# Optimization experiments

Measured on AMD Instinct MI355X. Metric: run time of the kernel, lower is better.

## Reference

```python
import jax, jax.numpy as jnp
import numpy as np

E, EMB, H, MUL = 100000, 64, 128, 64
SQRT3 = 1.7320508075688772
SQRT6 = 2.449489742783178
INV_SQRT2 = 0.7071067811865476  # path normalization: 2 paths feed 0e and 1o outputs


def setup_inputs() -> dict:
    key = jax.random.key(0)
    ks = jax.random.split(key, 10)
    d = {
        "emb": jax.random.normal(ks[0], (E, EMB), jnp.float32),
        "x1": jax.random.normal(ks[1], (E, 4 * MUL), jnp.float32),   # 64x0e + 64x1o
        "x2": jax.random.normal(ks[2], (E, 4), jnp.float32),          # 1x0e + 1x1o
        "W0": jax.random.normal(ks[3], (EMB, H), jnp.float32),
        "W1": jax.random.normal(ks[4], (H, H), jnp.float32),
    }
    for i, k in enumerate(ks[5:10]):
        d[f"P{i+1}"] = jax.random.normal(k, (H, MUL), jnp.float32)
    return d


def _forward(emb, x1, x2, W0, W1, P1, P2, P3, P4, P5):
    # MLP with 1/sqrt(fan_in) normalization (e3nn haiku MultiLayerPerceptron)
    h = jax.nn.silu(emb @ W0 / jnp.sqrt(jnp.float32(EMB)))
    h = jax.nn.silu(h @ W1 / jnp.sqrt(jnp.float32(H)))            # (E, H)
    inv = 1.0 / jnp.sqrt(jnp.float32(H))                           # w.shape[0]**-0.5
    # per-instruction path weights, shape (E, MUL): einsum('x...,x->...') batched
    w1, w2, w3, w4, w5 = (h @ P * inv for P in (P1, P2, P3, P4, P5))

    x1_0 = x1[:, :MUL]                                             # (E, MUL)    0e
    x1_1 = x1[:, MUL:].reshape(E, MUL, 3)                          # (E, MUL, 3) 1o
    x2_0 = x2[:, 0]                                                # (E,)        0e
    x2_1 = x2[:, 1:4]                                              # (E, 3)      1o

    # instruction 1: 0e x 0e -> 0e   (w3j = 1)
    # instruction 4: 1o x 1o -> 0e   (w3j = delta_ij / sqrt(3))
    out_0e = INV_SQRT2 * (
        w1 * x1_0 * x2_0[:, None]
        + w4 * jnp.einsum("eui,ei->eu", x1_1, x2_1) / SQRT3
    )                                                              # (E, MUL)
    # instruction 2: 1o x 0e -> 1o ; instruction 3: 0e x 1o -> 1o
    out_1o = INV_SQRT2 * (
        w2[:, :, None] * x1_1 * x2_0[:, None, None]
        + w3[:, :, None] * x1_0[:, :, None] * x2_1[:, None, :]
    )                                                              # (E, MUL, 3)
    # instruction 5: 1o x 1o -> 1e  (w3j = eps_ijk / sqrt(6))
    out_1e = w5[:, :, None] * jnp.cross(x1_1, x2_1[:, None, :]) / SQRT6

    return jnp.concatenate(
        [out_0e, out_1o.reshape(E, 3 * MUL), out_1e.reshape(E, 3 * MUL)], axis=-1
    )                                                              # (E, 448)


def reference(emb, x1, x2, W0, W1, P1, P2, P3, P4, P5):
    return _forward(emb, x1, x2, W0, W1, P1, P2, P3, P4, P5)
```

## Files before the change

kernel.cpp:

```cpp
#include <hip/hip_runtime.h>

#define E_TOT 100000

typedef _Float16 half8   __attribute__((ext_vector_type(8)));
typedef float    float4v __attribute__((ext_vector_type(4)));

__device__ __forceinline__ float silu_f(float x) {
    return x / (1.0f + __expf(-x));
}

__global__ void prep_weights(const float* __restrict__ W0,
                             const float* __restrict__ W1,
                             const float* __restrict__ P1,
                             const float* __restrict__ P2,
                             const float* __restrict__ P3,
                             const float* __restrict__ P4,
                             const float* __restrict__ P5,
                             _Float16* __restrict__ wf)
{
    int gid  = blockIdx.x * 256 + threadIdx.x;
    int j    = gid & 7;
    int lane = (gid >> 3) & 63;
    int krow = ((lane >> 4) << 3) + j;
    int ncol = lane & 15;
    float v;
    if (gid < 8192) {
        int kt = (gid >> 9) & 1, nt = gid >> 10;
        v = W0[(kt * 32 + krow) * 128 + nt * 16 + ncol];
    } else if (gid < 24576) {
        int rem = gid - 8192;
        int kt = (rem >> 9) & 3, nt = rem >> 11;
        v = W1[(kt * 32 + krow) * 128 + nt * 16 + ncol];
    } else {
        int rem = gid - 24576;
        int kt = (rem >> 9) & 3, nt = (rem >> 11) & 3, m = rem >> 13;
        const float* Pm = (m == 0) ? P1 : (m == 1) ? P2 : (m == 2) ? P3 : (m == 3) ? P4 : P5;
        v = Pm[(kt * 32 + krow) * 64 + nt * 16 + ncol];
    }
    wf[gid] = (_Float16)v;
}

__global__ __launch_bounds__(256, 4)
void tpmlp_main(const float* __restrict__ emb,
                const float* __restrict__ x1,
                const float* __restrict__ x2,
                const _Float16* __restrict__ wf,
                float* __restrict__ out)
{
    const float INV_SQRT_EMB = 0.125f;
    const float INV_SQRT_H   = 0.08838834764831845f;
    const float INV_SQRT3    = 0.5773502691896258f;
    const float INV_SQRT6    = 0.4082482904638631f;
    const float INV_SQRT2_C  = 0.7071067811865476f;

    __shared__ _Float16 s_h[64 * 136];

    const int tid  = threadIdx.x;
    const int lane = tid & 63;
    const int wv   = tid >> 6;
    const int l15  = lane & 15;
    const int lq   = lane >> 4;
    const int e0   = blockIdx.x * 64;

    const _Float16* __restrict__ W0f = wf;
    const _Float16* __restrict__ W1f = wf + 8192;
    const _Float16* __restrict__ Pf  = wf + 24576;

    half8 a0 = {0,0,0,0,0,0,0,0}, a1 = {0,0,0,0,0,0,0,0};
    {
        int row = e0 + wv * 16 + l15;
        if (row < E_TOT) {
            const float* er = emb + (size_t)row * 64 + lq * 8;
            float4v v0 = *(const float4v*)er;
            float4v v1 = *(const float4v*)(er + 4);
            float4v v2 = *(const float4v*)(er + 32);
            float4v v3 = *(const float4v*)(er + 36);
            #pragma unroll
            for (int t = 0; t < 4; ++t) { a0[t] = (_Float16)v0[t]; a0[4+t] = (_Float16)v1[t]; }
            #pragma unroll
            for (int t = 0; t < 4; ++t) { a1[t] = (_Float16)v2[t]; a1[4+t] = (_Float16)v3[t]; }
        }
    }

    #pragma unroll
    for (int nt = 0; nt < 8; ++nt) {
        float4v c = {0.f, 0.f, 0.f, 0.f};
        half8 b0 = *(const half8*)&W0f[((nt * 2 + 0) * 64 + lane) * 8];
        half8 b1 = *(const half8*)&W0f[((nt * 2 + 1) * 64 + lane) * 8];
        c = __builtin_amdgcn_mfma_f32_16x16x32_f16(a0, b0, c, 0, 0, 0);
        c = __builtin_amdgcn_mfma_f32_16x16x32_f16(a1, b1, c, 0, 0, 0);
        #pragma unroll
        for (int r = 0; r < 4; ++r)
            s_h[(wv * 16 + lq * 4 + r) * 136 + nt * 16 + l15] =
                (_Float16)silu_f(c[r] * INV_SQRT_EMB);
    }
    __syncthreads();

    half8 a2[4];
    #pragma unroll
    for (int kt = 0; kt < 4; ++kt)
        a2[kt] = *(const half8*)&s_h[(wv * 16 + l15) * 136 + kt * 32 + lq * 8];
    __syncthreads();

    #pragma unroll
    for (int nt = 0; nt < 8; ++nt) {
        float4v c = {0.f, 0.f, 0.f, 0.f};
        #pragma unroll
        for (int kt = 0; kt < 4; ++kt) {
            half8 b = *(const half8*)&W1f[((nt * 4 + kt) * 64 + lane) * 8];
            c = __builtin_amdgcn_mfma_f32_16x16x32_f16(a2[kt], b, c, 0, 0, 0);
        }
        #pragma unroll
        for (int r = 0; r < 4; ++r)
            s_h[(wv * 16 + lq * 4 + r) * 136 + nt * 16 + l15] =
                (_Float16)silu_f(c[r] * INV_SQRT_H);
    }
    __syncthreads();

    half8 a3[4];
    #pragma unroll
    for (int kt = 0; kt < 4; ++kt)
        a3[kt] = *(const half8*)&s_h[(wv * 16 + l15) * 136 + kt * 32 + lq * 8];

    float4v acc3[5][4];
    #pragma unroll
    for (int m = 0; m < 5; ++m)
        #pragma unroll
        for (int nt = 0; nt < 4; ++nt)
            acc3[m][nt] = (float4v){0.f, 0.f, 0.f, 0.f};

    #pragma unroll
    for (int m = 0; m < 5; ++m)
        #pragma unroll
        for (int nt = 0; nt < 4; ++nt)
            #pragma unroll
            for (int kt = 0; kt < 4; ++kt) {
                half8 b = *(const half8*)&Pf[((m * 16 + nt * 4 + kt) * 64 + lane) * 8];
                acc3[m][nt] = __builtin_amdgcn_mfma_f32_16x16x32_f16(a3[kt], b, acc3[m][nt], 0, 0, 0);
            }

    #pragma unroll
    for (int r = 0; r < 4; ++r) {
        int e = e0 + wv * 16 + lq * 4 + r;
        if (e < E_TOT) {
            const float* x1p = x1 + (size_t)e * 256;
            float4v x2v = *(const float4v*)(x2 + (size_t)e * 4);
            float x20 = x2v[0], b0 = x2v[1], b1 = x2v[2], b2 = x2v[3];
            float* op = out + (size_t)e * 448;
            #pragma unroll
            for (int nt = 0; nt < 4; ++nt) {
                int u = nt * 16 + l15;
                float w1 = acc3[0][nt][r] * INV_SQRT_H;
                float w2 = acc3[1][nt][r] * INV_SQRT_H;
                float w3 = acc3[2][nt][r] * INV_SQRT_H;
                float w4 = acc3[3][nt][r] * INV_SQRT_H;
                float w5 = acc3[4][nt][r] * INV_SQRT_H;

                float x10 = x1p[u];
                float a_0 = x1p[64 + 3 * u];
                float a_1 = x1p[65 + 3 * u];
                float a_2 = x1p[66 + 3 * u];

                float dot = a_0 * b0 + a_1 * b1 + a_2 * b2;

                op[u] = INV_SQRT2_C * (w1 * x10 * x20 + w4 * dot * INV_SQRT3);

                op[64 + 3 * u] = INV_SQRT2_C * (w2 * a_0 * x20 + w3 * x10 * b0);
                op[65 + 3 * u] = INV_SQRT2_C * (w2 * a_1 * x20 + w3 * x10 * b1);
                op[66 + 3 * u] = INV_SQRT2_C * (w2 * a_2 * x20 + w3 * x10 * b2);

                op[256 + 3 * u] = w5 * (a_1 * b2 - a_2 * b1) * INV_SQRT6;
                op[257 + 3 * u] = w5 * (a_2 * b0 - a_0 * b2) * INV_SQRT6;
                op[258 + 3 * u] = w5 * (a_0 * b1 - a_1 * b0) * INV_SQRT6;
            }
        }
    }
}

extern "C" void kernel_launch(void* const* d_in, const int* in_sizes, int n_in,
                              void* d_out, int out_size, void* d_ws, size_t ws_size,
                              hipStream_t stream) {
    const float* emb = (const float*)d_in[0];
    const float* x1  = (const float*)d_in[1];
    const float* x2  = (const float*)d_in[2];
    const float* W0  = (const float*)d_in[3];
    const float* W1  = (const float*)d_in[4];
    const float* P1  = (const float*)d_in[5];
    const float* P2  = (const float*)d_in[6];
    const float* P3  = (const float*)d_in[7];
    const float* P4  = (const float*)d_in[8];
    const float* P5  = (const float*)d_in[9];

    _Float16* wf = (_Float16*)d_ws;

    prep_weights<<<dim3(256), dim3(256), 0, stream>>>(W0, W1, P1, P2, P3, P4, P5, wf);
    tpmlp_main<<<dim3((E_TOT + 63) / 64), dim3(256), 0, stream>>>(
        emb, x1, x2, wf, (float*)d_out);
}
```

Measured before the change: 320.1 us.

## Use single-wave blocks over 32 rows, reuse B fragments, nontemporal output stores

Each block becomes one 64-lane wavefront handling two 16-row tiles. Every weight fragment loaded from global memory now feeds two MFMAs instead of one, and the P-stage accumulators are restructured per output column tile to reduce live registers. Output writes switch to nontemporal stores to avoid polluting cache. Bounds checks are removed; this relies on E being divisible by 32, which holds for 100000.

```diff
diff --git a/kernel.cpp b/kernel.cpp
--- a/kernel.cpp
+++ b/kernel.cpp
@@ -40,7 +40,7 @@
     wf[gid] = (_Float16)v;
 }
 
-__global__ __launch_bounds__(256, 4)
+__global__ __launch_bounds__(64, 4)
 void tpmlp_main(const float* __restrict__ emb,
                 const float* __restrict__ x1,
                 const float* __restrict__ x2,
@@ -53,108 +53,119 @@
     const float INV_SQRT6    = 0.4082482904638631f;
     const float INV_SQRT2_C  = 0.7071067811865476f;
 
-    __shared__ _Float16 s_h[64 * 136];
-
-    const int tid  = threadIdx.x;
-    const int lane = tid & 63;
-    const int wv   = tid >> 6;
+    __shared__ _Float16 s_h[32 * 136];
+
+    const int lane = threadIdx.x;
     const int l15  = lane & 15;
     const int lq   = lane >> 4;
-    const int e0   = blockIdx.x * 64;
+    const int e0   = blockIdx.x * 32;
 
     const _Float16* __restrict__ W0f = wf;
     const _Float16* __restrict__ W1f = wf + 8192;
     const _Float16* __restrict__ Pf  = wf + 24576;
 
-    half8 a0 = {0,0,0,0,0,0,0,0}, a1 = {0,0,0,0,0,0,0,0};
-    {
-        int row = e0 + wv * 16 + l15;
-        if (row < E_TOT) {
-            const float* er = emb + (size_t)row * 64 + lq * 8;
-            float4v v0 = *(const float4v*)er;
-            float4v v1 = *(const float4v*)(er + 4);
-            float4v v2 = *(const float4v*)(er + 32);
-            float4v v3 = *(const float4v*)(er + 36);
-            #pragma unroll
-            for (int t = 0; t < 4; ++t) { a0[t] = (_Float16)v0[t]; a0[4+t] = (_Float16)v1[t]; }
-            #pragma unroll
-            for (int t = 0; t < 4; ++t) { a1[t] = (_Float16)v2[t]; a1[4+t] = (_Float16)v3[t]; }
+    half8 a0[2], a1[2];
+    #pragma unroll
+    for (int t = 0; t < 2; ++t) {
+        const float* er = emb + (size_t)(e0 + t * 16 + l15) * 64 + lq * 8;
+        float4v v0 = *(const float4v*)er;
+        float4v v1 = *(const float4v*)(er + 4);
+        float4v v2 = *(const float4v*)(er + 32);
+        float4v v3 = *(const float4v*)(er + 36);
+        #pragma unroll
+        for (int q = 0; q < 4; ++q) {
+            a0[t][q] = (_Float16)v0[q]; a0[t][4 + q] = (_Float16)v1[q];
+            a1[t][q] = (_Float16)v2[q]; a1[t][4 + q] = (_Float16)v3[q];
         }
     }
 
     #pragma unroll
     for (int nt = 0; nt < 8; ++nt) {
-        float4v c = {0.f, 0.f, 0.f, 0.f};
         half8 b0 = *(const half8*)&W0f[((nt * 2 + 0) * 64 + lane) * 8];
         half8 b1 = *(const half8*)&W0f[((nt * 2 + 1) * 64 + lane) * 8];
-        c = __builtin_amdgcn_mfma_f32_16x16x32_f16(a0, b0, c, 0, 0, 0);
-        c = __builtin_amdgcn_mfma_f32_16x16x32_f16(a1, b1, c, 0, 0, 0);
-        #pragma unroll
-        for (int r = 0; r < 4; ++r)
-            s_h[(wv * 16 + lq * 4 + r) * 136 + nt * 16 + l15] =
-                (_Float16)silu_f(c[r] * INV_SQRT_EMB);
+        #pragma unroll
+        for (int t = 0; t < 2; ++t) {
+            float4v c = {0.f, 0.f, 0.f, 0.f};
+            c = __builtin_amdgcn_mfma_f32_16x16x32_f16(a0[t], b0, c, 0, 0, 0);
+            c = __builtin_amdgcn_mfma_f32_16x16x32_f16(a1[t], b1, c, 0, 0, 0);
+            #pragma unroll
+            for (int r = 0; r < 4; ++r)
+                s_h[(t * 16 + lq * 4 + r) * 136 + nt * 16 + l15] =
+                    (_Float16)silu_f(c[r] * INV_SQRT_EMB);
+        }
     }
     __syncthreads();
 
-    half8 a2[4];
-    #pragma unroll
-    for (int kt = 0; kt < 4; ++kt)
-        a2[kt] = *(const half8*)&s_h[(wv * 16 + l15) * 136 + kt * 32 + lq * 8];
+    half8 a2[2][4];
+    #pragma unroll
+    for (int t = 0; t < 2; ++t)
+        #pragma unroll
+        for (int kt = 0; kt < 4; ++kt)
+            a2[t][kt] = *(const half8*)&s_h[(t * 16 + l15) * 136 + kt * 32 + lq * 8];
     __syncthreads();
 
     #pragma unroll
     for (int nt = 0; nt < 8; ++nt) {
-        float4v c = {0.f, 0.f, 0.f, 0.f};
-        #pragma unroll
-        for (int kt = 0; kt < 4; ++kt) {
-            half8 b = *(const half8*)&W1f[((nt * 4 + kt) * 64 + lane) * 8];
-            c = __builtin_amdgcn_mfma_f32_16x16x32_f16(a2[kt], b, c, 0, 0, 0);
+        half8 b[4];
+        #pragma unroll
+        for (int kt = 0; kt < 4; ++kt)
+            b[kt] = *(const half8*)&W1f[((nt * 4 + kt) * 64 + lane) * 8];
+        #pragma unroll
+        for (int t = 0; t < 2; ++t) {
+            float4v c = {0.f, 0.f, 0.f, 0.f};
+            #pragma unroll
+            for (int kt = 0; kt < 4; ++kt)
+                c = __builtin_amdgcn_mfma_f32_16x16x32_f16(a2[t][kt], b[kt], c, 0, 0, 0);
+            #pragma unroll
+            for (int r = 0; r < 4; ++r)
+                s_h[(t * 16 + lq * 4 + r) * 136 + nt * 16 + l15] =
+                    (_Float16)silu_f(c[r] * INV_SQRT_H);
         }
-        #pragma unroll
-        for (int r = 0; r < 4; ++r)
-            s_h[(wv * 16 + lq * 4 + r) * 136 + nt * 16 + l15] =
-                (_Float16)silu_f(c[r] * INV_SQRT_H);
     }
     __syncthreads();
 
-    half8 a3[4];
-    #pragma unroll
-    for (int kt = 0; kt < 4; ++kt)
-        a3[kt] = *(const half8*)&s_h[(wv * 16 + l15) * 136 + kt * 32 + lq * 8];
-
-    float4v acc3[5][4];
-    #pragma unroll
-    for (int m = 0; m < 5; ++m)
-        #pragma unroll
-        for (int nt = 0; nt < 4; ++nt)
-            acc3[m][nt] = (float4v){0.f, 0.f, 0.f, 0.f};
-
-    #pragma unroll
-    for (int m = 0; m < 5; ++m)
-        #pragma unroll
-        for (int nt = 0; nt < 4; ++nt)
+    half8 a3[2][4];
+    #pragma unroll
+    for (int t = 0; t < 2; ++t)
+        #pragma unroll
+        for (int kt = 0; kt < 4; ++kt)
+            a3[t][kt] = *(const half8*)&s_h[(t * 16 + l15) * 136 + kt * 32 + lq * 8];
+
+    #pragma unroll
+    for (int nt = 0; nt < 4; ++nt) {
+        float4v acc[2][5];
+        #pragma unroll
+        for (int t = 0; t < 2; ++t)
+            #pragma unroll
+            for (int m = 0; m < 5; ++m)
+                acc[t][m] = (float4v){0.f, 0.f, 0.f, 0.f};
+
+        #pragma unroll
+        for (int m = 0; m < 5; ++m)
             #pragma unroll
             for (int kt = 0; kt < 4; ++kt) {
                 half8 b = *(const half8*)&Pf[((m * 16 + nt * 4 + kt) * 64 + lane) * 8];
-                acc3[m][nt] = __builtin_amdgcn_mfma_f32_16x16x32_f16(a3[kt], b, acc3[m][nt], 0, 0, 0);
+                #pragma unroll
+                for (int t = 0; t < 2; ++t)
+                    acc[t][m] = __builtin_amdgcn_mfma_f32_16x16x32_f16(a3[t][kt], b, acc[t][m], 0, 0, 0);
             }
 
-    #pragma unroll
-    for (int r = 0; r < 4; ++r) {
-        int e = e0 + wv * 16 + lq * 4 + r;
-        if (e < E_TOT) {
-            const float* x1p = x1 + (size_t)e * 256;
-            float4v x2v = *(const float4v*)(x2 + (size_t)e * 4);
-            float x20 = x2v[0], b0 = x2v[1], b1 = x2v[2], b2 = x2v[3];
-            float* op = out + (size_t)e * 448;
-            #pragma unroll
-            for (int nt = 0; nt < 4; ++nt) {
-                int u = nt * 16 + l15;
-                float w1 = acc3[0][nt][r] * INV_SQRT_H;
-                float w2 = acc3[1][nt][r] * INV_SQRT_H;
-                float w3 = acc3[2][nt][r] * INV_SQRT_H;
-                float w4 = acc3[3][nt][r] * INV_SQRT_H;
-                float w5 = acc3[4][nt][r] * INV_SQRT_H;
+        const int u = nt * 16 + l15;
+        #pragma unroll
+        for (int t = 0; t < 2; ++t)
+            #pragma unroll
+            for (int r = 0; r < 4; ++r) {
+                const int e = e0 + t * 16 + lq * 4 + r;
+                const float* x1p = x1 + (size_t)e * 256;
+                float4v x2v = *(const float4v*)(x2 + (size_t)e * 4);
+                float x20 = x2v[0], b0 = x2v[1], b1 = x2v[2], b2 = x2v[3];
+                float* op = out + (size_t)e * 448;
+
+                float w1 = acc[t][0][r] * INV_SQRT_H;
+                float w2 = acc[t][1][r] * INV_SQRT_H;
+                float w3 = acc[t][2][r] * INV_SQRT_H;
+                float w4 = acc[t][3][r] * INV_SQRT_H;
+                float w5 = acc[t][4][r] * INV_SQRT_H;
 
                 float x10 = x1p[u];
                 float a_0 = x1p[64 + 3 * u];
@@ -163,17 +174,23 @@
 
                 float dot = a_0 * b0 + a_1 * b1 + a_2 * b2;
 
-                op[u] = INV_SQRT2_C * (w1 * x10 * x20 + w4 * dot * INV_SQRT3);
-
-                op[64 + 3 * u] = INV_SQRT2_C * (w2 * a_0 * x20 + w3 * x10 * b0);
-                op[65 + 3 * u] = INV_SQRT2_C * (w2 * a_1 * x20 + w3 * x10 * b1);
-                op[66 + 3 * u] = INV_SQRT2_C * (w2 * a_2 * x20 + w3 * x10 * b2);
-
-                op[256 + 3 * u] = w5 * (a_1 * b2 - a_2 * b1) * INV_SQRT6;
-                op[257 + 3 * u] = w5 * (a_2 * b0 - a_0 * b2) * INV_SQRT6;
-                op[258 + 3 * u] = w5 * (a_0 * b1 - a_1 * b0) * INV_SQRT6;
+                __builtin_nontemporal_store(
+                    INV_SQRT2_C * (w1 * x10 * x20 + w4 * dot * INV_SQRT3), op + u);
+
+                __builtin_nontemporal_store(
+                    INV_SQRT2_C * (w2 * a_0 * x20 + w3 * x10 * b0), op + 64 + 3 * u);
+                __builtin_nontemporal_store(
+                    INV_SQRT2_C * (w2 * a_1 * x20 + w3 * x10 * b1), op + 65 + 3 * u);
+                __builtin_nontemporal_store(
+                    INV_SQRT2_C * (w2 * a_2 * x20 + w3 * x10 * b2), op + 66 + 3 * u);
+
+                __builtin_nontemporal_store(
+                    w5 * (a_1 * b2 - a_2 * b1) * INV_SQRT6, op + 256 + 3 * u);
+                __builtin_nontemporal_store(
+                    w5 * (a_2 * b0 - a_0 * b2) * INV_SQRT6, op + 257 + 3 * u);
+                __builtin_nontemporal_store(
+                    w5 * (a_0 * b1 - a_1 * b0) * INV_SQRT6, op + 258 + 3 * u);
             }
-        }
     }
 }
 
@@ -194,6 +211,6 @@
     _Float16* wf = (_Float16*)d_ws;
 
     prep_weights<<<dim3(256), dim3(256), 0, stream>>>(W0, W1, P1, P2, P3, P4, P5, wf);
-    tpmlp_main<<<dim3((E_TOT + 63) / 64), dim3(256), 0, stream>>>(
+    tpmlp_main<<<dim3((E_TOT + 31) / 32), dim3(64), 0, stream>>>(
         emb, x1, x2, wf, (float*)d_out);
 }
```

After: 388.2 us. 1.21x slower.

## Use single-wave blocks and interleave projection MFMAs with per-tile epilogue

Applied to the files above, without the earlier changes.

Blocks shrink from four waves over 64 rows to one wave over 16 rows, so barriers only synchronize a single wave and shared memory per block drops. The projection stage now computes the five weight tiles for one column slice and immediately applies the tensor-product epilogue, cutting live accumulators from 80 to 20 registers to ease register pressure and occupancy limits. x2 values are prefetched at kernel start. Bounds checks are removed, which is valid because 100000 divides by 16. The trade-off is four times as many blocks and per-wave reloads of the shared weight fragments.

```diff
diff --git a/kernel.cpp b/kernel.cpp
--- a/kernel.cpp
+++ b/kernel.cpp
@@ -40,7 +40,7 @@
     wf[gid] = (_Float16)v;
 }
 
-__global__ __launch_bounds__(256, 4)
+__global__ __launch_bounds__(64, 4)
 void tpmlp_main(const float* __restrict__ emb,
                 const float* __restrict__ x1,
                 const float* __restrict__ x2,
@@ -53,45 +53,46 @@
     const float INV_SQRT6    = 0.4082482904638631f;
     const float INV_SQRT2_C  = 0.7071067811865476f;
 
-    __shared__ _Float16 s_h[64 * 136];
+    __shared__ _Float16 s_h[16 * 136];
 
-    const int tid  = threadIdx.x;
-    const int lane = tid & 63;
-    const int wv   = tid >> 6;
+    const int lane = threadIdx.x;
     const int l15  = lane & 15;
     const int lq   = lane >> 4;
-    const int e0   = blockIdx.x * 64;
+    const int e0   = blockIdx.x * 16;
 
     const _Float16* __restrict__ W0f = wf;
     const _Float16* __restrict__ W1f = wf + 8192;
     const _Float16* __restrict__ Pf  = wf + 24576;
 
-    half8 a0 = {0,0,0,0,0,0,0,0}, a1 = {0,0,0,0,0,0,0,0};
+    float4v x2pre[4];
+    #pragma unroll
+    for (int r = 0; r < 4; ++r)
+        x2pre[r] = *(const float4v*)(x2 + (size_t)(e0 + lq * 4 + r) * 4);
+
+    half8 a0, a1;
     {
-        int row = e0 + wv * 16 + l15;
-        if (row < E_TOT) {
-            const float* er = emb + (size_t)row * 64 + lq * 8;
-            float4v v0 = *(const float4v*)er;
-            float4v v1 = *(const float4v*)(er + 4);
-            float4v v2 = *(const float4v*)(er + 32);
-            float4v v3 = *(const float4v*)(er + 36);
-            #pragma unroll
-            for (int t = 0; t < 4; ++t) { a0[t] = (_Float16)v0[t]; a0[4+t] = (_Float16)v1[t]; }
-            #pragma unroll
-            for (int t = 0; t < 4; ++t) { a1[t] = (_Float16)v2[t]; a1[4+t] = (_Float16)v3[t]; }
+        const float* er = emb + (size_t)(e0 + l15) * 64 + lq * 8;
+        float4v v0 = *(const float4v*)er;
+        float4v v1 = *(const float4v*)(er + 4);
+        float4v v2 = *(const float4v*)(er + 32);
+        float4v v3 = *(const float4v*)(er + 36);
+        #pragma unroll
+        for (int q = 0; q < 4; ++q) {
+            a0[q] = (_Float16)v0[q]; a0[4 + q] = (_Float16)v1[q];
+            a1[q] = (_Float16)v2[q]; a1[4 + q] = (_Float16)v3[q];
         }
     }
 
     #pragma unroll
     for (int nt = 0; nt < 8; ++nt) {
-        float4v c = {0.f, 0.f, 0.f, 0.f};
         half8 b0 = *(const half8*)&W0f[((nt * 2 + 0) * 64 + lane) * 8];
         half8 b1 = *(const half8*)&W0f[((nt * 2 + 1) * 64 + lane) * 8];
+        float4v c = {0.f, 0.f, 0.f, 0.f};
         c = __builtin_amdgcn_mfma_f32_16x16x32_f16(a0, b0, c, 0, 0, 0);
         c = __builtin_amdgcn_mfma_f32_16x16x32_f16(a1, b1, c, 0, 0, 0);
         #pragma unroll
         for (int r = 0; r < 4; ++r)
-            s_h[(wv * 16 + lq * 4 + r) * 136 + nt * 16 + l15] =
+            s_h[(lq * 4 + r) * 136 + nt * 16 + l15] =
                 (_Float16)silu_f(c[r] * INV_SQRT_EMB);
     }
     __syncthreads();
@@ -99,7 +100,7 @@
     half8 a2[4];
     #pragma unroll
     for (int kt = 0; kt < 4; ++kt)
-        a2[kt] = *(const half8*)&s_h[(wv * 16 + l15) * 136 + kt * 32 + lq * 8];
+        a2[kt] = *(const half8*)&s_h[l15 * 136 + kt * 32 + lq * 8];
     __syncthreads();
 
     #pragma unroll
@@ -112,7 +113,7 @@
         }
         #pragma unroll
         for (int r = 0; r < 4; ++r)
-            s_h[(wv * 16 + lq * 4 + r) * 136 + nt * 16 + l15] =
+            s_h[(lq * 4 + r) * 136 + nt * 16 + l15] =
                 (_Float16)silu_f(c[r] * INV_SQRT_H);
     }
     __syncthreads();
@@ -120,59 +121,53 @@
     half8 a3[4];
     #pragma unroll
     for (int kt = 0; kt < 4; ++kt)
-        a3[kt] = *(const half8*)&s_h[(wv * 16 + l15) * 136 + kt * 32 + lq * 8];
-
-    float4v acc3[5][4];
-    #pragma unroll
-    for (int m = 0; m < 5; ++m)
-        #pragma unroll
-        for (int nt = 0; nt < 4; ++nt)
-            acc3[m][nt] = (float4v){0.f, 0.f, 0.f, 0.f};
+        a3[kt] = *(const half8*)&s_h[l15 * 136 + kt * 32 + lq * 8];
 
     #pragma unroll
-    for (int m = 0; m < 5; ++m)
+    for (int nt = 0; nt < 4; ++nt) {
+        float4v acc[5];
         #pragma unroll
-        for (int nt = 0; nt < 4; ++nt)
+        for (int m = 0; m < 5; ++m)
+            acc[m] = (float4v){0.f, 0.f, 0.f, 0.f};
+
+        #pragma unroll
+        for (int m = 0; m < 5; ++m)
             #pragma unroll
             for (int kt = 0; kt < 4; ++kt) {
                 half8 b = *(const half8*)&Pf[((m * 16 + nt * 4 + kt) * 64 + lane) * 8];
-                acc3[m][nt] = __builtin_amdgcn_mfma_f32_16x16x32_f16(a3[kt], b, acc3[m][nt], 0, 0, 0);
+                acc[m] = __builtin_amdgcn_mfma_f32_16x16x32_f16(a3[kt], b, acc[m], 0, 0, 0);
             }
 
-    #pragma unroll
-    for (int r = 0; r < 4; ++r) {
-        int e = e0 + wv * 16 + lq * 4 + r;
-        if (e < E_TOT) {
+        const int u = nt * 16 + l15;
+        #pragma unroll
+        for (int r = 0; r < 4; ++r) {
+            const int e = e0 + lq * 4 + r;
             const float* x1p = x1 + (size_t)e * 256;
-            float4v x2v = *(const float4v*)(x2 + (size_t)e * 4);
-            float x20 = x2v[0], b0 = x2v[1], b1 = x2v[2], b2 = x2v[3];
+            float x20 = x2pre[r][0], b0 = x2pre[r][1], b1 = x2pre[r][2], b2 = x2pre[r][3];
             float* op = out + (size_t)e * 448;
-            #pragma unroll
-            for (int nt = 0; nt < 4; ++nt) {
-                int u = nt * 16 + l15;
-                float w1 = acc3[0][nt][r] * INV_SQRT_H;
-                float w2 = acc3[1][nt][r] * INV_SQRT_H;
-                float w3 = acc3[2][nt][r] * INV_SQRT_H;
-                float w4 = acc3[3][nt][r] * INV_SQRT_H;
-                float w5 = acc3[4][nt][r] * INV_SQRT_H;
 
-                float x10 = x1p[u];
-                float a_0 = x1p[64 + 3 * u];
-                float a_1 = x1p[65 + 3 * u];
-                float a_2 = x1p[66 + 3 * u];
+            float w1 = acc[0][r] * INV_SQRT_H;
+            float w2 = acc[1][r] * INV_SQRT_H;
+            float w3 = acc[2][r] * INV_SQRT_H;
+            float w4 = acc[3][r] * INV_SQRT_H;
+            float w5 = acc[4][r] * INV_SQRT_H;
 
-                float dot = a_0 * b0 + a_1 * b1 + a_2 * b2;
+            float x10 = x1p[u];
+            float a_0 = x1p[64 + 3 * u];
+            float a_1 = x1p[65 + 3 * u];
+            float a_2 = x1p[66 + 3 * u];
 
-                op[u] = INV_SQRT2_C * (w1 * x10 * x20 + w4 * dot * INV_SQRT3);
+            float dot = a_0 * b0 + a_1 * b1 + a_2 * b2;
 
-                op[64 + 3 * u] = INV_SQRT2_C * (w2 * a_0 * x20 + w3 * x10 * b0);
-                op[65 + 3 * u] = INV_SQRT2_C * (w2 * a_1 * x20 + w3 * x10 * b1);
-                op[66 + 3 * u] = INV_SQRT2_C * (w2 * a_2 * x20 + w3 * x10 * b2);
+            op[u] = INV_SQRT2_C * (w1 * x10 * x20 + w4 * dot * INV_SQRT3);
 
-                op[256 + 3 * u] = w5 * (a_1 * b2 - a_2 * b1) * INV_SQRT6;
-                op[257 + 3 * u] = w5 * (a_2 * b0 - a_0 * b2) * INV_SQRT6;
-                op[258 + 3 * u] = w5 * (a_0 * b1 - a_1 * b0) * INV_SQRT6;
-            }
+            op[64 + 3 * u] = INV_SQRT2_C * (w2 * a_0 * x20 + w3 * x10 * b0);
+            op[65 + 3 * u] = INV_SQRT2_C * (w2 * a_1 * x20 + w3 * x10 * b1);
+            op[66 + 3 * u] = INV_SQRT2_C * (w2 * a_2 * x20 + w3 * x10 * b2);
+
+            op[256 + 3 * u] = w5 * (a_1 * b2 - a_2 * b1) * INV_SQRT6;
+            op[257 + 3 * u] = w5 * (a_2 * b0 - a_0 * b2) * INV_SQRT6;
+            op[258 + 3 * u] = w5 * (a_0 * b1 - a_1 * b0) * INV_SQRT6;
         }
     }
 }
@@ -194,6 +189,6 @@
     _Float16* wf = (_Float16*)d_ws;
 
     prep_weights<<<dim3(256), dim3(256), 0, stream>>>(W0, W1, P1, P2, P3, P4, P5, wf);
-    tpmlp_main<<<dim3((E_TOT + 63) / 64), dim3(256), 0, stream>>>(
+    tpmlp_main<<<dim3((E_TOT + 15) / 16), dim3(64), 0, stream>>>(
         emb, x1, x2, wf, (float*)d_out);
 }
```

New measurement: 392.4 us. 1.23x slower.

## Transpose final MFMA so each lane owns one edge row and store with vector writes

Applied to the files above, without the earlier changes.

Swaps the A/B operands of the path-weight MFMAs so the accumulator layout puts one edge per lane with four consecutive channels. The epilogue can then read x1 and write the output with contiguous float4 accesses instead of strided scalar loads and stores. The normalization scales are folded into the fp16 weights during prep. The P-matmul loop is also restructured per column tile, which lowers accumulator register pressure. Risks are a small fp16 rounding change from pre-scaling the weights, and out-of-range rows now perform clamped redundant loads.

```diff
diff --git a/kernel.cpp b/kernel.cpp
--- a/kernel.cpp
+++ b/kernel.cpp
@@ -18,6 +18,7 @@
                              const float* __restrict__ P5,
                              _Float16* __restrict__ wf)
 {
+    const float INV_SQRT_H = 0.08838834764831845f;
     int gid  = blockIdx.x * 256 + threadIdx.x;
     int j    = gid & 7;
     int lane = (gid >> 3) & 63;
@@ -26,16 +27,16 @@
     float v;
     if (gid < 8192) {
         int kt = (gid >> 9) & 1, nt = gid >> 10;
-        v = W0[(kt * 32 + krow) * 128 + nt * 16 + ncol];
+        v = W0[(kt * 32 + krow) * 128 + nt * 16 + ncol] * 0.125f;
     } else if (gid < 24576) {
         int rem = gid - 8192;
         int kt = (rem >> 9) & 3, nt = rem >> 11;
-        v = W1[(kt * 32 + krow) * 128 + nt * 16 + ncol];
+        v = W1[(kt * 32 + krow) * 128 + nt * 16 + ncol] * INV_SQRT_H;
     } else {
         int rem = gid - 24576;
         int kt = (rem >> 9) & 3, nt = (rem >> 11) & 3, m = rem >> 13;
         const float* Pm = (m == 0) ? P1 : (m == 1) ? P2 : (m == 2) ? P3 : (m == 3) ? P4 : P5;
-        v = Pm[(kt * 32 + krow) * 64 + nt * 16 + ncol];
+        v = Pm[(kt * 32 + krow) * 64 + nt * 16 + ncol] * INV_SQRT_H;
     }
     wf[gid] = (_Float16)v;
 }
@@ -47,11 +48,9 @@
                 const _Float16* __restrict__ wf,
                 float* __restrict__ out)
 {
-    const float INV_SQRT_EMB = 0.125f;
-    const float INV_SQRT_H   = 0.08838834764831845f;
-    const float INV_SQRT3    = 0.5773502691896258f;
-    const float INV_SQRT6    = 0.4082482904638631f;
-    const float INV_SQRT2_C  = 0.7071067811865476f;
+    const float INV_SQRT3   = 0.5773502691896258f;
+    const float INV_SQRT6   = 0.4082482904638631f;
+    const float INV_SQRT2_C = 0.7071067811865476f;
 
     __shared__ _Float16 s_h[64 * 136];
 
@@ -62,37 +61,41 @@
     const int lq   = lane >> 4;
     const int e0   = blockIdx.x * 64;
 
+    const int erow  = e0 + wv * 16 + l15;
+    const bool valid = erow < E_TOT;
+    const int crow  = valid ? erow : (E_TOT - 1);
+
     const _Float16* __restrict__ W0f = wf;
     const _Float16* __restrict__ W1f = wf + 8192;
     const _Float16* __restrict__ Pf  = wf + 24576;
 
-    half8 a0 = {0,0,0,0,0,0,0,0}, a1 = {0,0,0,0,0,0,0,0};
+    const float4v x2v = *(const float4v*)(x2 + (size_t)crow * 4);
+
+    half8 a0, a1;
     {
-        int row = e0 + wv * 16 + l15;
-        if (row < E_TOT) {
-            const float* er = emb + (size_t)row * 64 + lq * 8;
-            float4v v0 = *(const float4v*)er;
-            float4v v1 = *(const float4v*)(er + 4);
-            float4v v2 = *(const float4v*)(er + 32);
-            float4v v3 = *(const float4v*)(er + 36);
-            #pragma unroll
-            for (int t = 0; t < 4; ++t) { a0[t] = (_Float16)v0[t]; a0[4+t] = (_Float16)v1[t]; }
-            #pragma unroll
-            for (int t = 0; t < 4; ++t) { a1[t] = (_Float16)v2[t]; a1[4+t] = (_Float16)v3[t]; }
+        const float* er = emb + (size_t)crow * 64 + lq * 8;
+        float4v v0 = *(const float4v*)er;
+        float4v v1 = *(const float4v*)(er + 4);
+        float4v v2 = *(const float4v*)(er + 32);
+        float4v v3 = *(const float4v*)(er + 36);
+        #pragma unroll
+        for (int q = 0; q < 4; ++q) {
+            a0[q] = (_Float16)v0[q]; a0[4 + q] = (_Float16)v1[q];
+            a1[q] = (_Float16)v2[q]; a1[4 + q] = (_Float16)v3[q];
         }
     }
 
     #pragma unroll
     for (int nt = 0; nt < 8; ++nt) {
-        float4v c = {0.f, 0.f, 0.f, 0.f};
         half8 b0 = *(const half8*)&W0f[((nt * 2 + 0) * 64 + lane) * 8];
         half8 b1 = *(const half8*)&W0f[((nt * 2 + 1) * 64 + lane) * 8];
+        float4v c = {0.f, 0.f, 0.f, 0.f};
         c = __builtin_amdgcn_mfma_f32_16x16x32_f16(a0, b0, c, 0, 0, 0);
         c = __builtin_amdgcn_mfma_f32_16x16x32_f16(a1, b1, c, 0, 0, 0);
         #pragma unroll
         for (int r = 0; r < 4; ++r)
             s_h[(wv * 16 + lq * 4 + r) * 136 + nt * 16 + l15] =
-                (_Float16)silu_f(c[r] * INV_SQRT_EMB);
+                (_Float16)silu_f(c[r]);
     }
     __syncthreads();
 
@@ -113,7 +116,7 @@
         #pragma unroll
         for (int r = 0; r < 4; ++r)
             s_h[(wv * 16 + lq * 4 + r) * 136 + nt * 16 + l15] =
-                (_Float16)silu_f(c[r] * INV_SQRT_H);
+                (_Float16)silu_f(c[r]);
     }
     __syncthreads();
 
@@ -122,56 +125,64 @@
     for (int kt = 0; kt < 4; ++kt)
         a3[kt] = *(const half8*)&s_h[(wv * 16 + l15) * 136 + kt * 32 + lq * 8];
 
-    float4v acc3[5][4];
-    #pragma unroll
-    for (int m = 0; m < 5; ++m)
-        #pragma unroll
-        for (int nt = 0; nt < 4; ++nt)
-            acc3[m][nt] = (float4v){0.f, 0.f, 0.f, 0.f};
-
-    #pragma unroll
-    for (int m = 0; m < 5; ++m)
-        #pragma unroll
-        for (int nt = 0; nt < 4; ++nt)
+    const float* x1r = x1 + (size_t)crow * 256;
+    float*       op  = out + (size_t)crow * 448;
+    const float x20 = x2v[0];
+    const float bi0 = x2v[1], bi1 = x2v[2], bi2 = x2v[3];
+
+    #pragma unroll
+    for (int nt = 0; nt < 4; ++nt) {
+        float4v x10v = *(const float4v*)(x1r + nt * 16 + 4 * lq);
+        float4v av0  = *(const float4v*)(x1r + 64 + nt * 48 + 12 * lq);
+        float4v av1  = *(const float4v*)(x1r + 64 + nt * 48 + 12 * lq + 4);
+        float4v av2  = *(const float4v*)(x1r + 64 + nt * 48 + 12 * lq + 8);
+
+        float4v acc[5];
+        #pragma unroll
+        for (int m = 0; m < 5; ++m)
+            acc[m] = (float4v){0.f, 0.f, 0.f, 0.f};
+        #pragma unroll
+        for (int m = 0; m < 5; ++m)
             #pragma unroll
             for (int kt = 0; kt < 4; ++kt) {
-                half8 b = *(const half8*)&Pf[((m * 16 + nt * 4 + kt) * 64 + lane) * 8];
-                acc3[m][nt] = __builtin_amdgcn_mfma_f32_16x16x32_f16(a3[kt], b, acc3[m][nt], 0, 0, 0);
+                half8 p = *(const half8*)&Pf[((m * 16 + nt * 4 + kt) * 64 + lane) * 8];
+                acc[m] = __builtin_amdgcn_mfma_f32_16x16x32_f16(p, a3[kt], acc[m], 0, 0, 0);
             }
 
-    #pragma unroll
-    for (int r = 0; r < 4; ++r) {
-        int e = e0 + wv * 16 + lq * 4 + r;
-        if (e < E_TOT) {
-            const float* x1p = x1 + (size_t)e * 256;
-            float4v x2v = *(const float4v*)(x2 + (size_t)e * 4);
-            float x20 = x2v[0], b0 = x2v[1], b1 = x2v[2], b2 = x2v[3];
-            float* op = out + (size_t)e * 448;
+        float af[12];
+        #pragma unroll
+        for (int q = 0; q < 4; ++q) {
+            af[q] = av0[q]; af[4 + q] = av1[q]; af[8 + q] = av2[q];
+        }
+
+        float4v o0;
+        #pragma unroll
+        for (int t = 0; t < 4; ++t) {
+            float dt = af[3 * t] * bi0 + af[3 * t + 1] * bi1 + af[3 * t + 2] * bi2;
+            o0[t] = INV_SQRT2_C * (acc[0][t] * x10v[t] * x20 + acc[3][t] * dt * INV_SQRT3);
+        }
+        if (valid)
+            *(float4v*)(op + nt * 16 + 4 * lq) = o0;
+
+        #pragma unroll
+        for (int q = 0; q < 3; ++q) {
+            float4v oo, oe;
             #pragma unroll
-            for (int nt = 0; nt < 4; ++nt) {
-                int u = nt * 16 + l15;
-                float w1 = acc3[0][nt][r] * INV_SQRT_H;
-                float w2 = acc3[1][nt][r] * INV_SQRT_H;
-                float w3 = acc3[2][nt][r] * INV_SQRT_H;
-                float w4 = acc3[3][nt][r] * INV_SQRT_H;
-                float w5 = acc3[4][nt][r] * INV_SQRT_H;
-
-                float x10 = x1p[u];
-                float a_0 = x1p[64 + 3 * u];
-                float a_1 = x1p[65 + 3 * u];
-                float a_2 = x1p[66 + 3 * u];
-
-                float dot = a_0 * b0 + a_1 * b1 + a_2 * b2;
-
-                op[u] = INV_SQRT2_C * (w1 * x10 * x20 + w4 * dot * INV_SQRT3);
-
-                op[64 + 3 * u] = INV_SQRT2_C * (w2 * a_0 * x20 + w3 * x10 * b0);
-                op[65 + 3 * u] = INV_SQRT2_C * (w2 * a_1 * x20 + w3 * x10 * b1);
-                op[66 + 3 * u] = INV_SQRT2_C * (w2 * a_2 * x20 + w3 * x10 * b2);
-
-                op[256 + 3 * u] = w5 * (a_1 * b2 - a_2 * b1) * INV_SQRT6;
-                op[257 + 3 * u] = w5 * (a_2 * b0 - a_0 * b2) * INV_SQRT6;
-                op[258 + 3 * u] = w5 * (a_0 * b1 - a_1 * b0) * INV_SQRT6;
+            for (int z = 0; z < 4; ++z) {
+                const int e2 = q * 4 + z;
+                const int t  = e2 / 3;
+                const int i  = e2 - 3 * t;
+                const float bii = (i == 0) ? bi0 : (i == 1) ? bi1 : bi2;
+                oo[z] = INV_SQRT2_C * (acc[1][t] * af[e2] * x20 +
+                                       acc[2][t] * x10v[t] * bii);
+                float cr = (i == 0) ? af[3 * t + 1] * bi2 - af[3 * t + 2] * bi1
+                         : (i == 1) ? af[3 * t + 2] * bi0 - af[3 * t + 0] * bi2
+                                    : af[3 * t + 0] * bi1 - af[3 * t + 1] * bi0;
+                oe[z] = acc[4][t] * cr * INV_SQRT6;
+            }
+            if (valid) {
+                *(float4v*)(op + 64  + nt * 48 + 12 * lq + 4 * q) = oo;
+                *(float4v*)(op + 256 + nt * 48 + 12 * lq + 4 * q) = oe;
             }
         }
     }
```

After: 365.9 us. 1.14x slower.
